# Optimization experiments

Measured on AMD Instinct MI355X. Metric: run time of the kernel, lower is better.

The kernel has to match this reference:

```python
import jax, jax.numpy as jnp
import numpy as np

B, S, HID = 2, 2048, 4096
NH, NKV, HD = 32, 8, 128
G = 128  # quant group size along input dim
NEG_INF = -1e9


def _rope_tables(key):
    inv_freq = 1.0 / (10000.0 ** (jnp.arange(0, HD, 2, dtype=jnp.float32) / HD))  # [HD/2]
    pos = jnp.arange(S, dtype=jnp.float32)
    ang = pos[:, None] * inv_freq[None, :]                  # [S, HD/2]
    emb = jnp.concatenate([ang, ang], axis=-1)              # [S, HD]
    cos = jnp.broadcast_to(jnp.cos(emb)[None], (B, S, HD))
    sin = jnp.broadcast_to(jnp.sin(emb)[None], (B, S, HD))
    return cos, sin


def setup_inputs() -> dict:
    key = jax.random.key(0)
    ks = jax.random.split(key, 10)
    hidden_states = jax.random.normal(ks[0], (B, S, HID), dtype=jnp.float32)
    cos, sin = _rope_tables(ks[1])
    causal = jnp.tril(jnp.ones((S, S), dtype=bool))
    attention_mask = jnp.broadcast_to(
        jnp.where(causal, 0.0, NEG_INF).astype(jnp.float32)[None, None], (B, 1, S, S))

    def qlinear(k, out_dim, in_dim):
        k1, k2 = jax.random.split(k)
        qw = jax.random.randint(k1, (out_dim, in_dim), 0, 16, dtype=jnp.int32)
        scale = jax.random.uniform(k2, (out_dim, in_dim // G), dtype=jnp.float32) * 0.01 + 0.001
        return qw, scale

    q_qw, q_scale = qlinear(ks[2], NH * HD, HID)
    k_qw, k_scale = qlinear(ks[3], NKV * HD, HID)
    v_qw, v_scale = qlinear(ks[4], NKV * HD, HID)
    o_qw, o_scale = qlinear(ks[5], HID, NH * HD)
    return dict(hidden_states=hidden_states, cos=cos, sin=sin,
                attention_mask=attention_mask,
                q_qw=q_qw, q_scale=q_scale, k_qw=k_qw, k_scale=k_scale,
                v_qw=v_qw, v_scale=v_scale, o_qw=o_qw, o_scale=o_scale)


def _dequant(qw, scale):
    # int4 codes in [0,16), zero-point 8, per-(row, input-group) scale
    out_dim, in_dim = qw.shape
    w = (qw.astype(jnp.float32) - 8.0).reshape(out_dim, in_dim // G, G)
    return (w * scale[:, :, None]).reshape(out_dim, in_dim)


def _rotate_half(x):
    x1, x2 = jnp.split(x, 2, axis=-1)
    return jnp.concatenate([-x2, x1], axis=-1)


def reference(hidden_states, cos, sin, attention_mask,
              q_qw, q_scale, k_qw, k_scale, v_qw, v_scale, o_qw, o_scale):
    scaling = HD ** -0.5
    Wq = _dequant(q_qw, q_scale)
    Wk = _dequant(k_qw, k_scale)
    Wv = _dequant(v_qw, v_scale)
    Wo = _dequant(o_qw, o_scale)

    q = jnp.einsum('bsh,oh->bso', hidden_states, Wq).reshape(B, S, NH, HD).transpose(0, 2, 1, 3)
    k = jnp.einsum('bsh,oh->bso', hidden_states, Wk).reshape(B, S, NKV, HD).transpose(0, 2, 1, 3)
    v = jnp.einsum('bsh,oh->bso', hidden_states, Wv).reshape(B, S, NKV, HD).transpose(0, 2, 1, 3)

    c = cos[:, None, :, :]  # [B,1,S,HD]
    s = sin[:, None, :, :]
    q = q * c + _rotate_half(q) * s
    k = k * c + _rotate_half(k) * s

    groups = NH // NKV
    k = jnp.repeat(k, groups, axis=1)  # [B,NH,S,HD]
    v = jnp.repeat(v, groups, axis=1)

    scores = jnp.einsum('bhsd,bhtd->bhst', q, k) * scaling + attention_mask
    probs = jax.nn.softmax(scores, axis=-1)
    ctx = jnp.einsum('bhst,bhtd->bhsd', probs, v)        # [B,NH,S,HD]
    ctx = ctx.transpose(0, 2, 1, 3).reshape(B, S, NH * HD)
    return jnp.einsum('bso,ho->bsh', ctx, Wo.T) if False else jnp.einsum('bsi,oi->bso', ctx, Wo)
```

## Files before the change

kernel.cpp:

```cpp
#include <hip/hip_runtime.h>
#include <hip/hip_bf16.h>

#define B_ 2
#define S_ 2048
#define HID_ 4096
#define NH_ 32
#define NKV_ 8
#define HD_ 128
#define T_ (B_*S_)

typedef __bf16 bf16;
typedef __bf16 bf16x8 __attribute__((ext_vector_type(8)));
typedef __bf16 bf16x4 __attribute__((ext_vector_type(4)));
typedef float f32x4 __attribute__((ext_vector_type(4)));

__device__ __forceinline__ void load_lds16(const void* g, void* l) {
  __builtin_amdgcn_global_load_lds((const __attribute__((address_space(1))) void*)g,
                                   (__attribute__((address_space(3))) void*)l, 16, 0, 0);
}

#define DPP_ROR(x, n) __int_as_float(__builtin_amdgcn_update_dpp( \
    __float_as_int(x), __float_as_int(x), 0x120 | (n), 0xf, 0xf, false))
__device__ __forceinline__ float red16_max(float x) {
  x = fmaxf(x, DPP_ROR(x, 1)); x = fmaxf(x, DPP_ROR(x, 2));
  x = fmaxf(x, DPP_ROR(x, 4)); x = fmaxf(x, DPP_ROR(x, 8));
  return x;
}
__device__ __forceinline__ float red16_sum(float x) {
  x += DPP_ROR(x, 1); x += DPP_ROR(x, 2);
  x += DPP_ROR(x, 4); x += DPP_ROR(x, 8);
  return x;
}

__global__ __launch_bounds__(256) void cvt_bf16_kernel(const float* __restrict__ in,
                                                       bf16* __restrict__ out, int n4) {
  int idx = blockIdx.x * 256 + threadIdx.x;
  if (idx >= n4) return;
  float4 v = ((const float4*)in)[idx];
  bf16x4 o;
  o.x = (bf16)v.x; o.y = (bf16)v.y; o.z = (bf16)v.z; o.w = (bf16)v.w;
  ((bf16x4*)out)[idx] = o;
}

__global__ __launch_bounds__(256) void dequant_kernel(const int* __restrict__ qw,
                                                      const float* __restrict__ scale,
                                                      bf16* __restrict__ out,
                                                      int OD, int ID) {
  int idx = blockIdx.x * 256 + threadIdx.x;
  int perRow = ID >> 3;
  int total = OD * perRow;
  if (idx >= total) return;
  int o = idx / perRow;
  int ic = idx - o * perRow;
  float s = scale[o * (ID >> 7) + ((ic * 8) >> 7)];
  const int* q = qw + (size_t)o * ID + ic * 8;
  int4 q0 = *(const int4*)q;
  int4 q1 = *(const int4*)(q + 4);
  bf16x8 r;
  r[0] = (bf16)((q0.x - 8) * s);
  r[1] = (bf16)((q0.y - 8) * s);
  r[2] = (bf16)((q0.z - 8) * s);
  r[3] = (bf16)((q0.w - 8) * s);
  r[4] = (bf16)((q1.x - 8) * s);
  r[5] = (bf16)((q1.y - 8) * s);
  r[6] = (bf16)((q1.z - 8) * s);
  r[7] = (bf16)((q1.w - 8) * s);
  *(bf16x8*)(out + (size_t)o * ID + ic * 8) = r;
}

__global__ __launch_bounds__(256) void gemm_bt_kernel(const bf16* __restrict__ A,
                                                      const bf16* __restrict__ Bm,
                                                      void* __restrict__ Cout,
                                                      int N, int K, int c_fp32) {
  __shared__ bf16 As[8192];
  __shared__ bf16 Bs[8192];
  int tid = threadIdx.x;
  int wave = tid >> 6, lane = tid & 63, quad = lane >> 4, l16 = lane & 15;
  int m0 = blockIdx.y * 128, n0 = blockIdx.x * 128;
  int wm = (wave >> 1) * 64, wn = (wave & 1) * 64;

  int srow = lane >> 3;
  int schunk = (lane & 7) ^ (srow & 7);
  const bf16* Ab[4];
  const bf16* Bb[4];
#pragma unroll
  for (int u = 0; u < 4; u++) {
    int t = wave + 4 * u;
    Ab[u] = A  + (size_t)(m0 + 8 * t + srow) * K + schunk * 8;
    Bb[u] = Bm + (size_t)(n0 + 8 * t + srow) * K + schunk * 8;
  }

  f32x4 acc[4][4];
#pragma unroll
  for (int mt = 0; mt < 4; mt++)
#pragma unroll
    for (int nt = 0; nt < 4; nt++) acc[mt][nt] = (f32x4){0.f, 0.f, 0.f, 0.f};

  for (int k0 = 0; k0 < K; k0 += 64) {
    __syncthreads();
#pragma unroll
    for (int u = 0; u < 4; u++) {
      int t = wave + 4 * u;
      load_lds16(Ab[u] + k0, (char*)As + t * 1024);
      load_lds16(Bb[u] + k0, (char*)Bs + t * 1024);
    }
    __syncthreads();
#pragma unroll
    for (int kk = 0; kk < 2; kk++) {
      bf16x8 af[4], bfr[4];
#pragma unroll
      for (int mt = 0; mt < 4; mt++) {
        int r = wm + mt * 16 + l16;
        af[mt] = *(const bf16x8*)((const char*)As + r * 128 + (((kk * 4 + quad) ^ (r & 7)) << 4));
      }
#pragma unroll
      for (int nt = 0; nt < 4; nt++) {
        int r = wn + nt * 16 + l16;
        bfr[nt] = *(const bf16x8*)((const char*)Bs + r * 128 + (((kk * 4 + quad) ^ (r & 7)) << 4));
      }
#pragma unroll
      for (int mt = 0; mt < 4; mt++)
#pragma unroll
        for (int nt = 0; nt < 4; nt++)
          acc[mt][nt] = __builtin_amdgcn_mfma_f32_16x16x32_bf16(af[mt], bfr[nt], acc[mt][nt], 0, 0, 0);
    }
  }

#pragma unroll
  for (int mt = 0; mt < 4; mt++)
#pragma unroll
    for (int nt = 0; nt < 4; nt++)
#pragma unroll
      for (int r = 0; r < 4; r++) {
        int rr = m0 + wm + mt * 16 + quad * 4 + r;
        int cc = n0 + wn + nt * 16 + l16;
        if (c_fp32) ((float*)Cout)[(size_t)rr * N + cc] = acc[mt][nt][r];
        else        ((bf16*)Cout)[(size_t)rr * N + cc] = (bf16)acc[mt][nt][r];
      }
}

__global__ __launch_bounds__(256) void gemm_rope_kernel(const bf16* __restrict__ A,
                                                        const bf16* __restrict__ Bm,
                                                        bf16* __restrict__ Out,
                                                        int N, int K,
                                                        const float* __restrict__ cosT,
                                                        const float* __restrict__ sinT,
                                                        float outscale) {
  __shared__ char smem[32768];
  bf16* As = (bf16*)smem;
  bf16* Bs = (bf16*)(smem + 16384);
  float* Ex = (float*)smem;
  int tid = threadIdx.x;
  int wave = tid >> 6, lane = tid & 63, quad = lane >> 4, l16 = lane & 15;
  int m0 = blockIdx.y * 128, n0 = blockIdx.x * 128;
  int wm = (wave >> 1) * 64, wn = (wave & 1) * 64;

  int srow = lane >> 3;
  int schunk = (lane & 7) ^ (srow & 7);
  const bf16* Ab[4];
  const bf16* Bb[4];
#pragma unroll
  for (int u = 0; u < 4; u++) {
    int t = wave + 4 * u;
    Ab[u] = A  + (size_t)(m0 + 8 * t + srow) * K + schunk * 8;
    Bb[u] = Bm + (size_t)(n0 + 8 * t + srow) * K + schunk * 8;
  }

  f32x4 acc[4][4];
#pragma unroll
  for (int mt = 0; mt < 4; mt++)
#pragma unroll
    for (int nt = 0; nt < 4; nt++) acc[mt][nt] = (f32x4){0.f, 0.f, 0.f, 0.f};

  for (int k0 = 0; k0 < K; k0 += 64) {
    __syncthreads();
#pragma unroll
    for (int u = 0; u < 4; u++) {
      int t = wave + 4 * u;
      load_lds16(Ab[u] + k0, (char*)As + t * 1024);
      load_lds16(Bb[u] + k0, (char*)Bs + t * 1024);
    }
    __syncthreads();
#pragma unroll
    for (int kk = 0; kk < 2; kk++) {
      bf16x8 af[4], bfr[4];
#pragma unroll
      for (int mt = 0; mt < 4; mt++) {
        int r = wm + mt * 16 + l16;
        af[mt] = *(const bf16x8*)((const char*)As + r * 128 + (((kk * 4 + quad) ^ (r & 7)) << 4));
      }
#pragma unroll
      for (int nt = 0; nt < 4; nt++) {
        int r = wn + nt * 16 + l16;
        bfr[nt] = *(const bf16x8*)((const char*)Bs + r * 128 + (((kk * 4 + quad) ^ (r & 7)) << 4));
      }
#pragma unroll
      for (int mt = 0; mt < 4; mt++)
#pragma unroll
        for (int nt = 0; nt < 4; nt++)
          acc[mt][nt] = __builtin_amdgcn_mfma_f32_16x16x32_bf16(af[mt], bfr[nt], acc[mt][nt], 0, 0, 0);
    }
  }

  int myb = tid * 17;
  int pb = (tid ^ 64) * 17;
#pragma unroll
  for (int mt = 0; mt < 4; mt++) {
    __syncthreads();
#pragma unroll
    for (int nt = 0; nt < 4; nt++)
#pragma unroll
      for (int r = 0; r < 4; r++)
        Ex[myb + nt * 4 + r] = acc[mt][nt][r];
    __syncthreads();
    int rowb = m0 + wm + mt * 16 + quad * 4;
#pragma unroll
    for (int nt = 0; nt < 4; nt++) {
      int cc = n0 + wn + nt * 16 + l16;
      int d = cc & 127;
#pragma unroll
      for (int r = 0; r < 4; r++) {
        int row = rowb + r;
        int t = row & (S_ - 1);
        float self = acc[mt][nt][r];
        float other = Ex[pb + nt * 4 + r];
        float c = cosT[t * 128 + d], s = sinT[t * 128 + d];
        float o = (d < 64) ? (self * c - other * s) : (self * c + other * s);
        Out[(size_t)row * N + cc] = (bf16)(o * outscale);
      }
    }
  }
}

template<int FUSE_ROPE, int C_FP32>
__global__ __launch_bounds__(512, 2) void gemm256_kernel(const bf16* __restrict__ A,
                                                         const bf16* __restrict__ Bm,
                                                         void* __restrict__ Cout,
                                                         int N, int K,
                                                         const float* __restrict__ cosT,
                                                         const float* __restrict__ sinT,
                                                         float outscale) {
  __shared__ char smem[131072];
  const int tid = threadIdx.x;
  const int wave = tid >> 6, lane = tid & 63, quad = lane >> 4, l16 = lane & 15;
  const int wm = (wave >> 2) * 128, wn = (wave & 3) * 64;

  int bid = blockIdx.y * gridDim.x + blockIdx.x;
  int cpx = (gridDim.x * gridDim.y) >> 3;
  int wgid = (bid & 7) * cpx + (bid >> 3);
  int m0 = (wgid / gridDim.x) * 256;
  int n0 = (wgid % gridDim.x) * 256;

  const int srow = wave * 16 + (lane >> 2);
  const int sc = (lane & 3) ^ ((lane >> 2) & 3) ^ quad;
  const bf16* aS0 = A  + (size_t)(m0 + srow) * K + sc * 8;
  const bf16* aS1 = A  + (size_t)(m0 + 128 + srow) * K + sc * 8;
  const bf16* bS0 = Bm + (size_t)(n0 + srow) * K + sc * 8;
  const bf16* bS1 = Bm + (size_t)(n0 + 128 + srow) * K + sc * 8;
  const int wl = wave * 1024;

  const int rslot = ((quad ^ (l16 & 3) ^ ((l16 >> 2) & 3)) << 4);
  const int aoff = (wm + l16) * 64 + rslot;
  const int boff = (wn + l16) * 64 + rslot;

  f32x4 acc[8][4];
#pragma unroll
  for (int mt = 0; mt < 8; mt++)
#pragma unroll
    for (int nt = 0; nt < 4; nt++) acc[mt][nt] = (f32x4){0.f, 0.f, 0.f, 0.f};

  load_lds16(aS0,      smem +     0 + wl); load_lds16(aS1,      smem +  8192 + wl);
  load_lds16(bS0,      smem + 32768 + wl); load_lds16(bS1,      smem + 40960 + wl);
  load_lds16(aS0 + 32, smem + 16384 + wl); load_lds16(aS1 + 32, smem + 24576 + wl);
  load_lds16(bS0 + 32, smem + 49152 + wl); load_lds16(bS1 + 32, smem + 57344 + wl);
  asm volatile("s_waitcnt vmcnt(0)" ::: "memory");
  __builtin_amdgcn_s_barrier();

  const int NT = K >> 6;
  for (int t = 0; t < NT; ++t) {
    const char* base = smem + (t & 1) * 65536;
    char* nb = smem + ((t & 1) ^ 1) * 65536;
    const int off = (t + 1) << 6;
    const bool more = (t + 1) < NT;
    bf16x8 afA[4], afB[4], bfr[4];

#pragma unroll
    for (int i = 0; i < 4; i++) afA[i] = *(const bf16x8*)(base + aoff + i * 1024);
#pragma unroll
    for (int i = 0; i < 4; i++) bfr[i] = *(const bf16x8*)(base + 32768 + boff + i * 1024);
    if (more) { load_lds16(aS0 + off, nb + wl); load_lds16(aS1 + off, nb + 8192 + wl); }
    __builtin_amdgcn_s_barrier();
    __builtin_amdgcn_s_setprio(1);
#pragma unroll
    for (int mt = 0; mt < 4; mt++)
#pragma unroll
      for (int nt = 0; nt < 4; nt++)
        acc[mt][nt] = __builtin_amdgcn_mfma_f32_16x16x32_bf16(afA[mt], bfr[nt], acc[mt][nt], 0, 0, 0);
    __builtin_amdgcn_s_setprio(0);
    __builtin_amdgcn_s_barrier();

#pragma unroll
    for (int i = 0; i < 4; i++) afB[i] = *(const bf16x8*)(base + aoff + (i + 4) * 1024);
    if (more) { load_lds16(bS0 + off, nb + 32768 + wl); load_lds16(bS1 + off, nb + 40960 + wl); }
    if (t == NT - 1) asm volatile("s_waitcnt vmcnt(0)" ::: "memory");
    else             asm volatile("s_waitcnt vmcnt(4)" ::: "memory");
    __builtin_amdgcn_s_barrier();
    __builtin_amdgcn_s_setprio(1);
#pragma unroll
    for (int mt = 0; mt < 4; mt++)
#pragma unroll
      for (int nt = 0; nt < 4; nt++)
        acc[mt + 4][nt] = __builtin_amdgcn_mfma_f32_16x16x32_bf16(afB[mt], bfr[nt], acc[mt + 4][nt], 0, 0, 0);
    __builtin_amdgcn_s_setprio(0);
    __builtin_amdgcn_s_barrier();

#pragma unroll
    for (int i = 0; i < 4; i++) afA[i] = *(const bf16x8*)(base + 16384 + aoff + i * 1024);
#pragma unroll
    for (int i = 0; i < 4; i++) bfr[i] = *(const bf16x8*)(base + 49152 + boff + i * 1024);
    if (more) { load_lds16(aS0 + off + 32, nb + 16384 + wl); load_lds16(aS1 + off + 32, nb + 24576 + wl); }
    __builtin_amdgcn_s_barrier();
    __builtin_amdgcn_s_setprio(1);
#pragma unroll
    for (int mt = 0; mt < 4; mt++)
#pragma unroll
      for (int nt = 0; nt < 4; nt++)
        acc[mt][nt] = __builtin_amdgcn_mfma_f32_16x16x32_bf16(afA[mt], bfr[nt], acc[mt][nt], 0, 0, 0);
    __builtin_amdgcn_s_setprio(0);
    __builtin_amdgcn_s_barrier();

#pragma unroll
    for (int i = 0; i < 4; i++) afB[i] = *(const bf16x8*)(base + 16384 + aoff + (i + 4) * 1024);
    if (more) {
      load_lds16(bS0 + off + 32, nb + 49152 + wl); load_lds16(bS1 + off + 32, nb + 57344 + wl);
      asm volatile("s_waitcnt vmcnt(4)" ::: "memory");
    }
    __builtin_amdgcn_s_barrier();
    __builtin_amdgcn_s_setprio(1);
#pragma unroll
    for (int mt = 0; mt < 4; mt++)
#pragma unroll
      for (int nt = 0; nt < 4; nt++)
        acc[mt + 4][nt] = __builtin_amdgcn_mfma_f32_16x16x32_bf16(afB[mt], bfr[nt], acc[mt + 4][nt], 0, 0, 0);
    __builtin_amdgcn_s_setprio(0);
    __builtin_amdgcn_s_barrier();
  }

  if (FUSE_ROPE) {
    float* Ex = (float*)smem;
    int myb = tid * 17;
    int pb = (tid ^ 64) * 17;
#pragma unroll
    for (int mt = 0; mt < 8; mt++) {
      __syncthreads();
#pragma unroll
      for (int nt = 0; nt < 4; nt++)
#pragma unroll
        for (int r = 0; r < 4; r++)
          Ex[myb + nt * 4 + r] = acc[mt][nt][r];
      __syncthreads();
      int rowb = m0 + wm + mt * 16 + quad * 4;
#pragma unroll
      for (int nt = 0; nt < 4; nt++) {
        int cc = n0 + wn + nt * 16 + l16;
        int d = cc & 127;
#pragma unroll
        for (int r = 0; r < 4; r++) {
          int row = rowb + r;
          int tp = row & (S_ - 1);
          float self = acc[mt][nt][r];
          float other = Ex[pb + nt * 4 + r];
          float c = cosT[tp * 128 + d], s = sinT[tp * 128 + d];
          float o = (d < 64) ? (self * c - other * s) : (self * c + other * s);
          ((bf16*)Cout)[(size_t)row * N + cc] = (bf16)(o * outscale);
        }
      }
    }
  } else {
#pragma unroll
    for (int mt = 0; mt < 8; mt++)
#pragma unroll
      for (int nt = 0; nt < 4; nt++)
#pragma unroll
        for (int r = 0; r < 4; r++) {
          int rr = m0 + wm + mt * 16 + quad * 4 + r;
          int cc = n0 + wn + nt * 16 + l16;
          if (C_FP32) ((float*)Cout)[(size_t)rr * N + cc] = acc[mt][nt][r];
          else        ((bf16*)Cout)[(size_t)rr * N + cc] = (bf16)acc[mt][nt][r];
        }
  }
}

__global__ __launch_bounds__(512, 4) void attn_kernel(const bf16* __restrict__ Qm,
                                                      const bf16* __restrict__ Km,
                                                      const bf16* __restrict__ VtG,
                                                      bf16* __restrict__ Cm) {
  __shared__ char sK[32768];
  __shared__ char sV[16384];
  __shared__ char sP[16384];
  int tid = threadIdx.x;
  int wave = tid >> 6, lane = tid & 63, quad = lane >> 4, l16 = lane & 15;
  int h = blockIdx.y, b = blockIdx.z;
  int kvh = h >> 2;

  const bf16* Kb[2];
  const bf16* Vb[2];
  {
    int r4 = lane >> 4, c16 = lane & 15;
    int r8 = lane >> 3, c8 = lane & 7;
#pragma unroll
    for (int u = 0; u < 2; u++) {
      int t = wave * 2 + u;
      int key = 4 * t + r4;
      int kc = c16 ^ (key & 7);
      Kb[u] = Km + (size_t)(b * S_ + key) * (NKV_ * HD_) + kvh * HD_ + kc * 8;
      int d = 8 * t + r8;
      int vc = c8 ^ (d & 7);
      Vb[u] = VtG + (size_t)(kvh * HD_ + d) * T_ + (size_t)b * S_ + vc * 8;
    }
  }

  for (int pass = 0; pass < 2; pass++) {
    int qt = pass ? ((S_ / 128 - 1) - (int)blockIdx.x) : (int)blockIdx.x;
    int q0 = qt * 128;
    int jend = q0 + 128;

#pragma unroll
    for (int u = 0; u < 2; u++)
      load_lds16(Kb[u], sK + (wave * 2 + u) * 1024);

    bf16x8 aQ[4];
    {
      int row = q0 + wave * 16 + l16;
      const bf16* qb = Qm + (size_t)(b * S_ + row) * (NH_ * HD_) + h * HD_;
#pragma unroll
      for (int kt = 0; kt < 4; kt++)
        aQ[kt] = *(const bf16x8*)(qb + kt * 32 + quad * 8);
    }

    float mcur[4], psum[4];
    f32x4 O[8];
#pragma unroll
    for (int r = 0; r < 4; r++) { mcur[r] = -1e30f; psum[r] = 0.f; }
#pragma unroll
    for (int n = 0; n < 8; n++) O[n] = (f32x4){0.f, 0.f, 0.f, 0.f};

    for (int j0 = 0; j0 < jend; j0 += 64) {
      int cur = (j0 >> 6) & 1;
      __syncthreads();
      if (j0 + 64 < jend) {
#pragma unroll
        for (int u = 0; u < 2; u++)
          load_lds16(Kb[u] + (size_t)(j0 + 64) * (NKV_ * HD_),
                     sK + (1 - cur) * 16384 + (wave * 2 + u) * 1024);
      }
#pragma unroll
      for (int u = 0; u < 2; u++)
        load_lds16(Vb[u] + j0, sV + (wave * 2 + u) * 1024);

      bool active = (j0 <= q0 + wave * 16 + 15);

      if (active) {
        const char* Kc = sK + cur * 16384;
        f32x4 sc[4];
#pragma unroll
        for (int nt = 0; nt < 4; nt++) sc[nt] = (f32x4){0.f, 0.f, 0.f, 0.f};
#pragma unroll
        for (int kt = 0; kt < 4; kt++) {
          bf16x8 bk[4];
#pragma unroll
          for (int nt = 0; nt < 4; nt++) {
            int key = nt * 16 + l16;
            bk[nt] = *(const bf16x8*)(Kc + key * 256 + (((kt * 4 + quad) ^ (key & 7)) << 4));
          }
#pragma unroll
          for (int nt = 0; nt < 4; nt++)
            sc[nt] = __builtin_amdgcn_mfma_f32_16x16x32_bf16(aQ[kt], bk[nt], sc[nt], 0, 0, 0);
        }

        int rowb = q0 + wave * 16 + quad * 4;
        if (j0 + 63 > q0 + wave * 16) {
#pragma unroll
          for (int nt = 0; nt < 4; nt++) {
            int col = j0 + nt * 16 + l16;
#pragma unroll
            for (int r = 0; r < 4; r++)
              if (col > rowb + r) sc[nt][r] = -1e9f;
          }
        }

        float vmax[4];
#pragma unroll
        for (int r = 0; r < 4; r++)
          vmax[r] = fmaxf(fmaxf(sc[0][r], sc[1][r]), fmaxf(sc[2][r], sc[3][r]));
        int nd = 0;
#pragma unroll
        for (int r = 0; r < 4; r++) nd |= (vmax[r] > mcur[r] + 8.f) ? 1 : 0;
        if (__any(nd)) {
          float al[4];
#pragma unroll
          for (int r = 0; r < 4; r++) {
            float rm = red16_max(vmax[r]);
            float mnew = fmaxf(mcur[r], rm);
            al[r] = exp2f(mcur[r] - mnew);
            mcur[r] = mnew;
            psum[r] *= al[r];
          }
#pragma unroll
          for (int n = 0; n < 8; n++)
#pragma unroll
            for (int r = 0; r < 4; r++) O[n][r] *= al[r];
        }
#pragma unroll
        for (int nt = 0; nt < 4; nt++)
#pragma unroll
          for (int r = 0; r < 4; r++)
            sc[nt][r] = exp2f(sc[nt][r] - mcur[r]);
#pragma unroll
        for (int r = 0; r < 4; r++)
          psum[r] += (sc[0][r] + sc[1][r]) + (sc[2][r] + sc[3][r]);

        char* Pw = sP + wave * 2048;
#pragma unroll
        for (int nt = 0; nt < 4; nt++) {
          int key = nt * 16 + l16;
#pragma unroll
          for (int r = 0; r < 4; r++) {
            int m = quad * 4 + r;
            *(bf16*)(Pw + m * 128 + ((((key >> 3) ^ (2 * quad)) & 7) << 4) + (key & 7) * 2) =
                (bf16)sc[nt][r];
          }
        }
      }

      __syncthreads();

      if (active) {
        char* Pw = sP + wave * 2048;
#pragma unroll
        for (int kt = 0; kt < 2; kt++) {
          bf16x8 ap = *(const bf16x8*)(Pw + l16 * 128 +
                      ((((kt * 4 + quad) ^ (2 * ((l16 >> 2) & 3))) & 7) << 4));
#pragma unroll
          for (int nt = 0; nt < 8; nt++) {
            int d = nt * 16 + l16;
            bf16x8 bv = *(const bf16x8*)(sV + d * 128 + (((kt * 4 + quad) ^ (d & 7)) << 4));
            O[nt] = __builtin_amdgcn_mfma_f32_16x16x32_bf16(ap, bv, O[nt], 0, 0, 0);
          }
        }
      }
    }

    float linv[4];
#pragma unroll
    for (int r = 0; r < 4; r++) linv[r] = 1.0f / red16_sum(psum[r]);
#pragma unroll
    for (int nt = 0; nt < 8; nt++)
#pragma unroll
      for (int r = 0; r < 4; r++) {
        int row = q0 + wave * 16 + quad * 4 + r;
        Cm[(size_t)(b * S_ + row) * (NH_ * HD_) + h * HD_ + nt * 16 + l16] =
            (bf16)(O[nt][r] * linv[r]);
      }
  }
}

extern "C" void kernel_launch(void* const* d_in, const int* in_sizes, int n_in,
                              void* d_out, int out_size, void* d_ws, size_t ws_size,
                              hipStream_t stream) {
  const float* hidden = (const float*)d_in[0];
  const float* cosT   = (const float*)d_in[1];
  const float* sinT   = (const float*)d_in[2];
  const int*   q_qw = (const int*)d_in[4];
  const float* q_sc = (const float*)d_in[5];
  const int*   k_qw = (const int*)d_in[6];
  const float* k_sc = (const float*)d_in[7];
  const int*   v_qw = (const int*)d_in[8];
  const float* v_sc = (const float*)d_in[9];
  const int*   o_qw = (const int*)d_in[10];
  const float* o_sc = (const float*)d_in[11];

  const size_t MB = 1024 * 1024;
  char* ws = (char*)d_ws;
  bf16* Xb  = (bf16*)(ws);
  bf16* Wb  = (bf16*)(ws + 32 * MB);
  bf16* Qm  = (bf16*)(ws + 64 * MB);
  bf16* Km  = (bf16*)(ws + 96 * MB);
  bf16* VtG = (bf16*)(ws + 104 * MB);
  bf16* Cm  = Xb;

  cvt_bf16_kernel<<<(T_ * HID_ / 4 + 255) / 256, 256, 0, stream>>>(hidden, Xb, T_ * HID_ / 4);

  const float qscale = (float)(0.08838834764831845 * 1.4426950408889634);

  dequant_kernel<<<(4096 * 512 + 255) / 256, 256, 0, stream>>>(q_qw, q_sc, Wb, 4096, 4096);
  gemm256_kernel<1, 0><<<dim3(16, 16), 512, 0, stream>>>(Xb, Wb, Qm, 4096, 4096,
                                                         cosT, sinT, qscale);

  dequant_kernel<<<(1024 * 512 + 255) / 256, 256, 0, stream>>>(k_qw, k_sc, Wb, 1024, 4096);
  gemm_rope_kernel<<<dim3(8, 32), 256, 0, stream>>>(Xb, Wb, Km, 1024, 4096, cosT, sinT, 1.0f);

  dequant_kernel<<<(1024 * 512 + 255) / 256, 256, 0, stream>>>(v_qw, v_sc, Wb, 1024, 4096);
  gemm_bt_kernel<<<dim3(32, 8), 256, 0, stream>>>(Wb, Xb, VtG, 4096, 4096, 0);

  attn_kernel<<<dim3(8, NH_, B_), 512, 0, stream>>>(Qm, Km, VtG, Cm);

  dequant_kernel<<<(4096 * 512 + 255) / 256, 256, 0, stream>>>(o_qw, o_sc, Wb, 4096, 4096);
  gemm256_kernel<0, 1><<<dim3(16, 16), 512, 0, stream>>>(Cm, Wb, d_out, 4096, 4096,
                                                         nullptr, nullptr, 1.0f);
}
```

Measured before the change: 800.4 us.

## Deepen GEMM LDS pipeline to four-slot ring with extra prefetch stage

Restructures the GEMM main loop's LDS staging from two 64-wide double buffers into a 4-slot ring of 32-wide K half-tiles for A and B. The prologue now issues three half-tiles, and each iteration keeps two stages in flight, using vmcnt(8) waits. The goal is to hide more global-to-LDS latency behind the MFMA work. The cost is more outstanding loads and trickier wait accounting, where an off-by-one count could cause a race.

```diff
diff --git a/kernel.cpp b/kernel.cpp
--- a/kernel.cpp
+++ b/kernel.cpp
@@ -269,26 +269,42 @@
 #pragma unroll
     for (int nt = 0; nt < 4; nt++) acc[mt][nt] = (f32x4){0.f, 0.f, 0.f, 0.f};
 
-  load_lds16(aS0,      smem +     0 + wl); load_lds16(aS1,      smem +  8192 + wl);
-  load_lds16(bS0,      smem + 32768 + wl); load_lds16(bS1,      smem + 40960 + wl);
-  load_lds16(aS0 + 32, smem + 16384 + wl); load_lds16(aS1 + 32, smem + 24576 + wl);
-  load_lds16(bS0 + 32, smem + 49152 + wl); load_lds16(bS1 + 32, smem + 57344 + wl);
-  asm volatile("s_waitcnt vmcnt(0)" ::: "memory");
+  load_lds16(aS0,      smem + 0 * 16384 + wl);
+  load_lds16(aS1,      smem + 0 * 16384 + 8192 + wl);
+  load_lds16(bS0,      smem + 65536 + 0 * 16384 + wl);
+  load_lds16(bS1,      smem + 65536 + 0 * 16384 + 8192 + wl);
+  load_lds16(aS0 + 32, smem + 1 * 16384 + wl);
+  load_lds16(aS1 + 32, smem + 1 * 16384 + 8192 + wl);
+  load_lds16(bS0 + 32, smem + 65536 + 1 * 16384 + wl);
+  load_lds16(bS1 + 32, smem + 65536 + 1 * 16384 + 8192 + wl);
+  load_lds16(aS0 + 64, smem + 2 * 16384 + wl);
+  load_lds16(aS1 + 64, smem + 2 * 16384 + 8192 + wl);
+  load_lds16(bS0 + 64, smem + 65536 + 2 * 16384 + wl);
+  load_lds16(bS1 + 64, smem + 65536 + 2 * 16384 + 8192 + wl);
+  asm volatile("s_waitcnt vmcnt(8)" ::: "memory");
   __builtin_amdgcn_s_barrier();
 
   const int NT = K >> 6;
   for (int t = 0; t < NT; ++t) {
-    const char* base = smem + (t & 1) * 65536;
-    char* nb = smem + ((t & 1) ^ 1) * 65536;
-    const int off = (t + 1) << 6;
-    const bool more = (t + 1) < NT;
+    const char* A0 = smem + (((2 * t) & 3) << 14);
+    const char* A1 = smem + (((2 * t + 1) & 3) << 14);
+    const char* B0 = A0 + 65536;
+    const char* B1 = A1 + 65536;
+    char* dA1n = smem + (((2 * t + 3) & 3) << 14);
+    char* dB1n = dA1n + 65536;
+    char* dA0n = smem + (((2 * t) & 3) << 14);
+    char* dB0n = dA0n + 65536;
+    const int offn1 = (t + 1) * 64 + 32;
+    const int offn2 = (t + 2) * 64;
+    const bool st1 = (t + 1) < NT;
+    const bool st2 = (t + 2) < NT;
     bf16x8 afA[4], afB[4], bfr[4];
 
 #pragma unroll
-    for (int i = 0; i < 4; i++) afA[i] = *(const bf16x8*)(base + aoff + i * 1024);
-#pragma unroll
-    for (int i = 0; i < 4; i++) bfr[i] = *(const bf16x8*)(base + 32768 + boff + i * 1024);
-    if (more) { load_lds16(aS0 + off, nb + wl); load_lds16(aS1 + off, nb + 8192 + wl); }
+    for (int i = 0; i < 4; i++) afA[i] = *(const bf16x8*)(A0 + aoff + i * 1024);
+#pragma unroll
+    for (int i = 0; i < 4; i++) bfr[i] = *(const bf16x8*)(B0 + boff + i * 1024);
+    if (st1) { load_lds16(aS0 + offn1, dA1n + wl); load_lds16(aS1 + offn1, dA1n + 8192 + wl); }
     __builtin_amdgcn_s_barrier();
     __builtin_amdgcn_s_setprio(1);
 #pragma unroll
@@ -300,10 +316,10 @@
     __builtin_amdgcn_s_barrier();
 
 #pragma unroll
-    for (int i = 0; i < 4; i++) afB[i] = *(const bf16x8*)(base + aoff + (i + 4) * 1024);
-    if (more) { load_lds16(bS0 + off, nb + 32768 + wl); load_lds16(bS1 + off, nb + 40960 + wl); }
-    if (t == NT - 1) asm volatile("s_waitcnt vmcnt(0)" ::: "memory");
-    else             asm volatile("s_waitcnt vmcnt(4)" ::: "memory");
+    for (int i = 0; i < 4; i++) afB[i] = *(const bf16x8*)(A0 + aoff + (i + 4) * 1024);
+    if (st1) { load_lds16(bS0 + offn1, dB1n + wl); load_lds16(bS1 + offn1, dB1n + 8192 + wl); }
+    if (st1) asm volatile("s_waitcnt vmcnt(8)" ::: "memory");
+    else     asm volatile("s_waitcnt vmcnt(0)" ::: "memory");
     __builtin_amdgcn_s_barrier();
     __builtin_amdgcn_s_setprio(1);
 #pragma unroll
@@ -315,10 +331,10 @@
     __builtin_amdgcn_s_barrier();
 
 #pragma unroll
-    for (int i = 0; i < 4; i++) afA[i] = *(const bf16x8*)(base + 16384 + aoff + i * 1024);
-#pragma unroll
-    for (int i = 0; i < 4; i++) bfr[i] = *(const bf16x8*)(base + 49152 + boff + i * 1024);
-    if (more) { load_lds16(aS0 + off + 32, nb + 16384 + wl); load_lds16(aS1 + off + 32, nb + 24576 + wl); }
+    for (int i = 0; i < 4; i++) afA[i] = *(const bf16x8*)(A1 + aoff + i * 1024);
+#pragma unroll
+    for (int i = 0; i < 4; i++) bfr[i] = *(const bf16x8*)(B1 + boff + i * 1024);
+    if (st2) { load_lds16(aS0 + offn2, dA0n + wl); load_lds16(aS1 + offn2, dA0n + 8192 + wl); }
     __builtin_amdgcn_s_barrier();
     __builtin_amdgcn_s_setprio(1);
 #pragma unroll
@@ -330,9 +346,11 @@
     __builtin_amdgcn_s_barrier();
 
 #pragma unroll
-    for (int i = 0; i < 4; i++) afB[i] = *(const bf16x8*)(base + 16384 + aoff + (i + 4) * 1024);
-    if (more) {
-      load_lds16(bS0 + off + 32, nb + 49152 + wl); load_lds16(bS1 + off + 32, nb + 57344 + wl);
+    for (int i = 0; i < 4; i++) afB[i] = *(const bf16x8*)(A1 + aoff + (i + 4) * 1024);
+    if (st2) {
+      load_lds16(bS0 + offn2, dB0n + wl); load_lds16(bS1 + offn2, dB0n + 8192 + wl);
+      asm volatile("s_waitcnt vmcnt(8)" ::: "memory");
+    } else if (st1) {
       asm volatile("s_waitcnt vmcnt(4)" ::: "memory");
     }
     __builtin_amdgcn_s_barrier();
```

Result: no change. 800.9 us (+0.1%).

## Restructure GEMM main loop into 4-stage half-K LDS ring with register prefetch

Applied to the files above, without the earlier changes.

Replaces the double-buffered 64-wide K tile with a four-slot ring of 32-wide K half-tiles, issuing global-to-LDS loads three half-steps ahead. Each half-step now runs all 32 MFMAs per wave, with the next A fragments and B fragments read from LDS into registers around the compute. Barriers per iteration drop from eight to two. The aim is to hide LDS and global latency better and cut synchronisation. The cost is more live registers (aE, aO, b), which risks lower occupancy or spills.

```diff
diff --git a/kernel.cpp b/kernel.cpp
--- a/kernel.cpp
+++ b/kernel.cpp
@@ -269,81 +269,93 @@
 #pragma unroll
     for (int nt = 0; nt < 4; nt++) acc[mt][nt] = (f32x4){0.f, 0.f, 0.f, 0.f};
 
-  load_lds16(aS0,      smem +     0 + wl); load_lds16(aS1,      smem +  8192 + wl);
-  load_lds16(bS0,      smem + 32768 + wl); load_lds16(bS1,      smem + 40960 + wl);
-  load_lds16(aS0 + 32, smem + 16384 + wl); load_lds16(aS1 + 32, smem + 24576 + wl);
-  load_lds16(bS0 + 32, smem + 49152 + wl); load_lds16(bS1 + 32, smem + 57344 + wl);
-  asm volatile("s_waitcnt vmcnt(0)" ::: "memory");
+  bf16x8 aE[8], aO[8], b[4];
+
+#pragma unroll
+  for (int h = 0; h < 3; h++) {
+    char* base = smem + (h << 14);
+    int koff = h * 32;
+    load_lds16(aS0 + koff, base + wl);
+    load_lds16(aS1 + koff, base + 8192 + wl);
+    load_lds16(bS0 + koff, base + 65536 + wl);
+    load_lds16(bS1 + koff, base + 65536 + 8192 + wl);
+  }
+  asm volatile("s_waitcnt vmcnt(8)" ::: "memory");
   __builtin_amdgcn_s_barrier();
+#pragma unroll
+  for (int i = 0; i < 8; i++) aE[i] = *(const bf16x8*)(smem + aoff + i * 1024);
+#pragma unroll
+  for (int n = 0; n < 4; n++) b[n] = *(const bf16x8*)(smem + 65536 + boff + n * 1024);
 
   const int NT = K >> 6;
   for (int t = 0; t < NT; ++t) {
-    const char* base = smem + (t & 1) * 65536;
-    char* nb = smem + ((t & 1) ^ 1) * 65536;
-    const int off = (t + 1) << 6;
-    const bool more = (t + 1) < NT;
-    bf16x8 afA[4], afB[4], bfr[4];
-
-#pragma unroll
-    for (int i = 0; i < 4; i++) afA[i] = *(const bf16x8*)(base + aoff + i * 1024);
-#pragma unroll
-    for (int i = 0; i < 4; i++) bfr[i] = *(const bf16x8*)(base + 32768 + boff + i * 1024);
-    if (more) { load_lds16(aS0 + off, nb + wl); load_lds16(aS1 + off, nb + 8192 + wl); }
-    __builtin_amdgcn_s_barrier();
-    __builtin_amdgcn_s_setprio(1);
-#pragma unroll
-    for (int mt = 0; mt < 4; mt++)
-#pragma unroll
-      for (int nt = 0; nt < 4; nt++)
-        acc[mt][nt] = __builtin_amdgcn_mfma_f32_16x16x32_bf16(afA[mt], bfr[nt], acc[mt][nt], 0, 0, 0);
-    __builtin_amdgcn_s_setprio(0);
-    __builtin_amdgcn_s_barrier();
-
-#pragma unroll
-    for (int i = 0; i < 4; i++) afB[i] = *(const bf16x8*)(base + aoff + (i + 4) * 1024);
-    if (more) { load_lds16(bS0 + off, nb + 32768 + wl); load_lds16(bS1 + off, nb + 40960 + wl); }
-    if (t == NT - 1) asm volatile("s_waitcnt vmcnt(0)" ::: "memory");
-    else             asm volatile("s_waitcnt vmcnt(4)" ::: "memory");
-    __builtin_amdgcn_s_barrier();
-    __builtin_amdgcn_s_setprio(1);
-#pragma unroll
-    for (int mt = 0; mt < 4; mt++)
-#pragma unroll
-      for (int nt = 0; nt < 4; nt++)
-        acc[mt + 4][nt] = __builtin_amdgcn_mfma_f32_16x16x32_bf16(afB[mt], bfr[nt], acc[mt + 4][nt], 0, 0, 0);
-    __builtin_amdgcn_s_setprio(0);
-    __builtin_amdgcn_s_barrier();
-
-#pragma unroll
-    for (int i = 0; i < 4; i++) afA[i] = *(const bf16x8*)(base + 16384 + aoff + i * 1024);
-#pragma unroll
-    for (int i = 0; i < 4; i++) bfr[i] = *(const bf16x8*)(base + 49152 + boff + i * 1024);
-    if (more) { load_lds16(aS0 + off + 32, nb + 16384 + wl); load_lds16(aS1 + off + 32, nb + 24576 + wl); }
-    __builtin_amdgcn_s_barrier();
-    __builtin_amdgcn_s_setprio(1);
-#pragma unroll
-    for (int mt = 0; mt < 4; mt++)
-#pragma unroll
-      for (int nt = 0; nt < 4; nt++)
-        acc[mt][nt] = __builtin_amdgcn_mfma_f32_16x16x32_bf16(afA[mt], bfr[nt], acc[mt][nt], 0, 0, 0);
-    __builtin_amdgcn_s_setprio(0);
-    __builtin_amdgcn_s_barrier();
-
-#pragma unroll
-    for (int i = 0; i < 4; i++) afB[i] = *(const bf16x8*)(base + 16384 + aoff + (i + 4) * 1024);
-    if (more) {
-      load_lds16(bS0 + off + 32, nb + 49152 + wl); load_lds16(bS1 + off + 32, nb + 57344 + wl);
-      asm volatile("s_waitcnt vmcnt(4)" ::: "memory");
-    }
-    __builtin_amdgcn_s_barrier();
-    __builtin_amdgcn_s_setprio(1);
-#pragma unroll
-    for (int mt = 0; mt < 4; mt++)
-#pragma unroll
-      for (int nt = 0; nt < 4; nt++)
-        acc[mt + 4][nt] = __builtin_amdgcn_mfma_f32_16x16x32_bf16(afB[mt], bfr[nt], acc[mt + 4][nt], 0, 0, 0);
-    __builtin_amdgcn_s_setprio(0);
-    __builtin_amdgcn_s_barrier();
+    {
+      if (t < NT - 1) {
+        char* base = smem + (((2 * t + 3) & 3) << 14);
+        int koff = (t + 1) * 64 + 32;
+        load_lds16(aS0 + koff, base + wl);
+        load_lds16(aS1 + koff, base + 8192 + wl);
+        load_lds16(bS0 + koff, base + 65536 + wl);
+        load_lds16(bS1 + koff, base + 65536 + 8192 + wl);
+        asm volatile("s_waitcnt vmcnt(8)" ::: "memory");
+      } else {
+        asm volatile("s_waitcnt vmcnt(0)" ::: "memory");
+      }
+      asm volatile("s_waitcnt lgkmcnt(0)" ::: "memory");
+      __builtin_amdgcn_s_barrier();
+      const char* nA = smem + (((2 * t + 1) & 3) << 14);
+#pragma unroll
+      for (int i = 0; i < 8; i++) aO[i] = *(const bf16x8*)(nA + aoff + i * 1024);
+      __builtin_amdgcn_sched_barrier(0);
+      __builtin_amdgcn_s_setprio(1);
+#pragma unroll
+      for (int mt = 0; mt < 8; mt++)
+#pragma unroll
+        for (int nt = 0; nt < 4; nt++)
+          acc[mt][nt] = __builtin_amdgcn_mfma_f32_16x16x32_bf16(aE[mt], b[nt], acc[mt][nt], 0, 0, 0);
+      __builtin_amdgcn_s_setprio(0);
+#pragma unroll
+      for (int n = 0; n < 4; n++) b[n] = *(const bf16x8*)(nA + 65536 + boff + n * 1024);
+    }
+
+    {
+      if (t < NT - 2) {
+        char* base = smem + (((2 * t) & 3) << 14);
+        int koff = (t + 2) * 64;
+        load_lds16(aS0 + koff, base + wl);
+        load_lds16(aS1 + koff, base + 8192 + wl);
+        load_lds16(bS0 + koff, base + 65536 + wl);
+        load_lds16(bS1 + koff, base + 65536 + 8192 + wl);
+        asm volatile("s_waitcnt vmcnt(8)" ::: "memory");
+      } else if (t == NT - 2) {
+        asm volatile("s_waitcnt vmcnt(4)" ::: "memory");
+      }
+      asm volatile("s_waitcnt lgkmcnt(0)" ::: "memory");
+      __builtin_amdgcn_s_barrier();
+      if (t < NT - 1) {
+        const char* nA = smem + (((2 * t + 2) & 3) << 14);
+#pragma unroll
+        for (int i = 0; i < 8; i++) aE[i] = *(const bf16x8*)(nA + aoff + i * 1024);
+        __builtin_amdgcn_sched_barrier(0);
+        __builtin_amdgcn_s_setprio(1);
+#pragma unroll
+        for (int mt = 0; mt < 8; mt++)
+#pragma unroll
+          for (int nt = 0; nt < 4; nt++)
+            acc[mt][nt] = __builtin_amdgcn_mfma_f32_16x16x32_bf16(aO[mt], b[nt], acc[mt][nt], 0, 0, 0);
+        __builtin_amdgcn_s_setprio(0);
+#pragma unroll
+        for (int n = 0; n < 4; n++) b[n] = *(const bf16x8*)(nA + 65536 + boff + n * 1024);
+      } else {
+        __builtin_amdgcn_s_setprio(1);
+#pragma unroll
+        for (int mt = 0; mt < 8; mt++)
+#pragma unroll
+          for (int nt = 0; nt < 4; nt++)
+            acc[mt][nt] = __builtin_amdgcn_mfma_f32_16x16x32_bf16(aO[mt], b[nt], acc[mt][nt], 0, 0, 0);
+        __builtin_amdgcn_s_setprio(0);
+      }
+    }
   }
 
   if (FUSE_ROPE) {
```

Result: slower. 1.715 ms (+114.3%).
